# Kernel tuning notes

Hardware: AMD Instinct MI355X
Metric: run time of the kernel (lower is better)

The kernel has to match this reference:

```python
import jax, jax.numpy as jnp
import numpy as np

N = 50000      # nodes
E = 800000     # edges (before self-loops)
NG = 64        # graphs
H, C = 4, 32   # heads, out channels per head
D = 128        # feature dim == H*C
GS, K = 4, 3   # grid_size, spline_order
NB = GS + K    # number of B-spline bases = 7
NC = 10        # classes
L = 3          # gnn layers

# uniform KAN grid over [-1,1] extended by spline_order on each side
GRID = jnp.arange(-K, GS + K + 1, dtype=jnp.float32) * (2.0 / GS) - 1.0  # [GS+2K+1]


def b_splines(x, grid, k):
    # x: [N, in] -> bases: [N, in, GS+k] via Cox-de Boor recursion
    xe = x[..., None]
    bases = ((xe >= grid[:-1]) & (xe < grid[1:])).astype(x.dtype)
    for p in range(1, k + 1):
        left = (xe - grid[:-(p + 1)]) / (grid[p:-1] - grid[:-(p + 1)]) * bases[..., :-1]
        right = (grid[p + 1:] - xe) / (grid[p + 1:] - grid[1:-p]) * bases[..., 1:]
        bases = left + right
    return bases


def kan_linear(x, base_w, spline_w, scaler):
    # efficient-kan: silu(x)@base_w.T + b_splines(x) contracted with scaled spline weights
    base = jax.nn.silu(x) @ base_w.T
    bs = b_splines(x, GRID, K)                      # [N, in, NB]
    sw = spline_w * scaler[..., None]               # [out, in, NB]
    return base + jnp.einsum('nib,oib->no', bs, sw)


def gat_layer(x, src, dst, base_w, spline_w, scaler, att_src, att_dst, bias):
    n = x.shape[0]
    h = kan_linear(x, base_w, spline_w, scaler).reshape(n, H, C)
    a_src = jnp.sum(h * att_src, axis=-1)           # [N, H]
    a_dst = jnp.sum(h * att_dst, axis=-1)           # [N, H]
    e = jax.nn.leaky_relu(a_src[src] + a_dst[dst], 0.2)  # [Etot, H]
    # segment softmax over incoming edges of each destination node
    m = jax.ops.segment_max(e, dst, num_segments=n)
    ex = jnp.exp(e - m[dst])
    s = jax.ops.segment_sum(ex, dst, num_segments=n)
    alpha = ex / (s[dst] + 1e-16)                   # [Etot, H]
    msg = h[src] * alpha[..., None]                 # [Etot, H, C]
    out = jax.ops.segment_sum(msg, dst, num_segments=n)
    return out.reshape(n, H * C) + bias


def setup_inputs() -> dict:
    key = jax.random.key(0)
    ks = jax.random.split(key, 16)
    inp = {
        'x': jax.random.normal(ks[0], (N, D), dtype=jnp.float32),
        'edge_index': jax.random.randint(ks[1], (2, E), 0, N, dtype=jnp.int32),
        'batch': jnp.sort(jax.random.randint(ks[2], (N,), 0, NG, dtype=jnp.int32)),
        # stacked per-layer GAT+KAN params (all layers are [128 -> 128])
        'base_w': jax.random.normal(ks[3], (L, D, D), dtype=jnp.float32) * 0.05,
        'spline_w': jax.random.normal(ks[4], (L, D, D, NB), dtype=jnp.float32) * 0.05,
        'scaler': jax.random.normal(ks[5], (L, D, D), dtype=jnp.float32) * 0.3 + 1.0,
        'att_src': jax.random.normal(ks[6], (L, H, C), dtype=jnp.float32) * 0.1,
        'att_dst': jax.random.normal(ks[7], (L, H, C), dtype=jnp.float32) * 0.1,
        'bias': jnp.zeros((L, H * C), dtype=jnp.float32),
        # readout KANLinear [128 -> 10]
        'ro_base_w': jax.random.normal(ks[8], (NC, D), dtype=jnp.float32) * 0.05,
        'ro_spline_w': jax.random.normal(ks[9], (NC, D, NB), dtype=jnp.float32) * 0.05,
        'ro_scaler': jax.random.normal(ks[10], (NC, D), dtype=jnp.float32) * 0.3 + 1.0,
    }
    return inp


def reference(x, edge_index, batch, base_w, spline_w, scaler, att_src, att_dst, bias,
              ro_base_w, ro_spline_w, ro_scaler):
    # PyG GATConv default: add self-loops
    loops = jnp.arange(N, dtype=edge_index.dtype)
    src = jnp.concatenate([edge_index[0], loops])
    dst = jnp.concatenate([edge_index[1], loops])
    h = x
    for i in range(L):
        h = gat_layer(h, src, dst, base_w[i], spline_w[i], scaler[i],
                      att_src[i], att_dst[i], bias[i])
        h = jax.nn.silu(h)  # dropout is identity in eval mode
    pooled = jax.ops.segment_sum(h, batch, num_segments=NG)   # global_add_pool [NG, D]
    logits = kan_linear(pooled, ro_base_w, ro_spline_w, ro_scaler)
    return jax.nn.log_softmax(logits, axis=1)
```

## Files before the change

### kernel.cpp

```cpp
#include <hip/hip_runtime.h>
#include <math.h>

#define NN 50000
#define EE 800000
#define ETOT (EE + NN)
#define NGR 64
#define DD 128
#define NCL 10

#define NBUK 128
#define BNODES 391
#define P1CH 3321
#define P2CAP 8704

typedef __attribute__((ext_vector_type(16))) float float16_t;
typedef __attribute__((ext_vector_type(8)))  __bf16 bf16x8;

__device__ __forceinline__ float siluf(float x){ return x / (1.f + __expf(-x)); }

__device__ __forceinline__ unsigned f2bf(float f){
  union { float f; unsigned u; } v; v.f = f;
  unsigned r = v.u + 0x7fffu + ((v.u >> 16) & 1u);
  return (r >> 16) & 0xffffu;
}

__device__ __forceinline__ void kan_feats(float x, float* f8){
  f8[0] = siluf(x);
  float u = 2.f*x + 5.f;
  int cell = -1;
  float n0=0.f,n1=0.f,n2=0.f,n3=0.f;
  if (u >= 0.f && u < 10.f){
    cell = (int)u;
    float t = u - (float)cell;
    float t2 = t*t, t3 = t2*t;
    float omt = 1.f - t;
    const float s6 = 1.f/6.f;
    n0 = t3*s6;
    n1 = s6*(1.f + 3.f*t + 3.f*t2 - 3.f*t3);
    n2 = s6*(4.f - 6.f*t2 + 3.f*t3);
    n3 = omt*omt*omt*s6;
  }
#pragma unroll
  for (int j=0;j<7;++j){
    int k = cell - j;
    float v = (k==0)?n0:((k==1)?n1:((k==2)?n2:((k==3)?n3:0.f)));
    f8[1+j] = v;
  }
}

__device__ __forceinline__ int4 kan_feats_pack(float x){
  unsigned sbf = f2bf(siluf(x));
  float u = 2.f*x + 5.f;
  bool valid = (u >= 0.f) && (u < 10.f);
  float uc = valid ? u : 0.f;
  int cell = (int)uc;
  float t = uc - (float)cell;
  float t2 = t*t, t3 = t2*t, omt = 1.f - t;
  const float s6 = 1.f/6.f;
  float n0 = t3*s6;
  float n1 = s6*(1.f + 3.f*t + 3.f*t2 - 3.f*t3);
  float n2 = s6*(4.f - 6.f*t2 + 3.f*t3);
  float n3 = omt*omt*omt*s6;
  unsigned p0=f2bf(n0), p1=f2bf(n1), p2=f2bf(n2), p3=f2bf(n3);
  unsigned long long P = ((unsigned long long)(p1 | (p0<<16)) << 32)
                       |  (unsigned long long)(p3 | (p2<<16));
  int sh = cell*16 - 48;
  unsigned long long shl    = P << (sh & 63);
  unsigned long long shrhi  = P >> ((64 - sh) & 63);
  unsigned long long shllo2 = P << ((sh - 64) & 63);
  unsigned long long shrlo  = P >> ((-sh) & 63);
  unsigned long long F0, F1;
  if (sh < 0)       { F0 = shrlo; F1 = 0ull; }
  else if (sh < 64) { F0 = shl;   F1 = (sh==0)? 0ull : shrhi; }
  else              { F0 = 0ull;  F1 = shllo2; }
  if (!valid){ F0 = 0ull; F1 = 0ull; }
  unsigned w0 = ((unsigned)(F0 & 0xffffull) << 16) | sbf;
  unsigned w1 = (unsigned)((F0 >> 16) & 0xffffffffull);
  unsigned w2 = (unsigned)((F0 >> 48) & 0xffffull) | (((unsigned)(F1 & 0xffffull)) << 16);
  unsigned w3 = (unsigned)((F1 >> 16) & 0xffffffffull);
  return make_int4((int)w0,(int)w1,(int)w2,(int)w3);
}

__global__ void hist_kernel(const int* __restrict__ ei, int* __restrict__ deg){
  int e = blockIdx.x*256 + threadIdx.x;
  if (e >= ETOT) return;
  int dst = (e < EE) ? ei[EE + e] : (e - EE);
  atomicAdd(&deg[dst], 1);
}

__global__ void scan1_kernel(const int* __restrict__ deg, int* __restrict__ offs, int* __restrict__ part){
  __shared__ int sh[256];
  int tid = threadIdx.x;
  int i = blockIdx.x*256 + tid;
  int v = (i < NN) ? deg[i] : 0;
  sh[tid] = v; __syncthreads();
  for (int o=1;o<256;o<<=1){
    int t2 = (tid >= o) ? sh[tid - o] : 0;
    __syncthreads();
    sh[tid] += t2;
    __syncthreads();
  }
  int incl = sh[tid];
  if (i < NN) offs[i] = incl - v;
  if (tid == 255) part[blockIdx.x] = incl;
}

__global__ void scan2_kernel(int* __restrict__ part, int nb){
  __shared__ int sh[256];
  int tid = threadIdx.x;
  int v = (tid < nb) ? part[tid] : 0;
  sh[tid] = v; __syncthreads();
  for (int o=1;o<256;o<<=1){
    int t2 = (tid >= o) ? sh[tid - o] : 0;
    __syncthreads();
    sh[tid] += t2;
    __syncthreads();
  }
  if (tid < nb) part[tid] = sh[tid] - v;
}

__global__ void scan3_kernel(int* __restrict__ offs, const int* __restrict__ part, int* __restrict__ cursor){
  int i = blockIdx.x*256 + threadIdx.x;
  if (i >= NN) return;
  int o = offs[i] + part[blockIdx.x];
  offs[i] = o;
  cursor[i] = o;
}

__global__ void binit_kernel(const int* __restrict__ offs, int* __restrict__ bcur){
  int b = threadIdx.x;
  if (b < NBUK) bcur[b] = offs[b*BNODES];
}

__global__ __launch_bounds__(256) void binpass_kernel(const int* __restrict__ ei,
                                                      int* __restrict__ bcur,
                                                      unsigned* __restrict__ tmp){
  __shared__ int cnt[NBUK], lexcl[NBUK], gbase[NBUK], lcur[NBUK];
  __shared__ int sc[NBUK];
  __shared__ unsigned entries[P1CH + 7];
  const int t = threadIdx.x;
  const int e0 = blockIdx.x * P1CH;
  int e1 = e0 + P1CH; if (e1 > ETOT) e1 = ETOT;
  const int total = e1 - e0;

  if (t < NBUK){ cnt[t] = 0; lcur[t] = 0; }
  __syncthreads();

  unsigned myE[14]; int myB[14]; int myN = 0;
  for (int e = e0 + t; e < e1; e += 256){
    int src, dst;
    if (e < EE){ src = ei[e]; dst = ei[EE + e]; } else { src = e - EE; dst = src; }
    int b = dst / BNODES;
    int dl = dst - b*BNODES;
    myE[myN] = ((unsigned)b << 25) | ((unsigned)dl << 16) | (unsigned)src;
    myB[myN] = b;
    myN++;
    atomicAdd(&cnt[b], 1);
  }
  __syncthreads();

  if (t < NBUK) sc[t] = cnt[t];
  __syncthreads();
  for (int o=1;o<NBUK;o<<=1){
    int v = 0;
    if (t < NBUK && t >= o) v = sc[t - o];
    __syncthreads();
    if (t < NBUK) sc[t] += v;
    __syncthreads();
  }
  if (t < NBUK) lexcl[t] = sc[t] - cnt[t];
  __syncthreads();

  if (t < NBUK && cnt[t] > 0) gbase[t] = atomicAdd(&bcur[t], cnt[t]);
  __syncthreads();

  for (int k=0;k<myN;++k){
    int b = myB[k];
    int r = lexcl[b] + atomicAdd(&lcur[b], 1);
    entries[r] = myE[k];
  }
  __syncthreads();

  for (int s = t; s < total; s += 256){
    unsigned en = entries[s];
    int b = en >> 25;
    int pos = gbase[b] + (s - lexcl[b]);
    tmp[pos] = en;
  }
}

__global__ __launch_bounds__(256) void scatter_kernel(const unsigned* __restrict__ tmp,
                                                      const int* __restrict__ offs,
                                                      int* __restrict__ cursor,
                                                      int* __restrict__ csr){
  __shared__ unsigned ebuf[P2CAP];
  __shared__ unsigned sbuf[P2CAP];
  __shared__ int dcnt[BNODES+1], dscan[BNODES+1], dcur[BNODES+1];
  __shared__ int sA[512], sB[512];
  const int t = threadIdx.x;
  const int b = blockIdx.x;
  const int lo = b * BNODES;
  const int start = offs[lo];
  const int end = (b < NBUK-1) ? offs[lo + BNODES] : ETOT;
  const int cnt = end - start;

  if (cnt > P2CAP){
    for (int i = t; i < cnt; i += 256){
      unsigned en = tmp[start + i];
      int node = lo + (int)((en >> 16) & 0x1FF);
      int pos = atomicAdd(&cursor[node], 1);
      csr[pos] = (int)(en & 0xFFFF);
    }
    return;
  }

  for (int i = t; i < cnt; i += 256) ebuf[i] = tmp[start + i];
  for (int i = t; i < BNODES+1; i += 256){ dcnt[i] = 0; dcur[i] = 0; }
  __syncthreads();
  for (int i = t; i < cnt; i += 256){
    int dl = (ebuf[i] >> 16) & 0x1FF;
    atomicAdd(&dcnt[dl], 1);
  }
  __syncthreads();

  sA[t]       = (t       < BNODES+1) ? dcnt[t]       : 0;
  sA[t + 256] = (t + 256 < BNODES+1) ? dcnt[t + 256] : 0;
  __syncthreads();
  int* sp = sA; int* dp = sB;
  for (int o=1;o<512;o<<=1){
    dp[t]       = sp[t]       + ((t       >= o) ? sp[t - o]       : 0);
    dp[t + 256] = sp[t + 256] + ((t + 256 >= o) ? sp[t + 256 - o] : 0);
    __syncthreads();
    int* tpp = sp; sp = dp; dp = tpp;
  }
  if (t       < BNODES+1) dscan[t]       = sp[t]       - dcnt[t];
  if (t + 256 < BNODES+1) dscan[t + 256] = sp[t + 256] - dcnt[t + 256];
  __syncthreads();

  for (int i = t; i < cnt; i += 256){
    unsigned en = ebuf[i];
    int dl = (en >> 16) & 0x1FF;
    int r = dscan[dl] + atomicAdd(&dcur[dl], 1);
    sbuf[r] = en & 0xFFFFu;
  }
  __syncthreads();
  for (int i = t; i < cnt; i += 256) csr[start + i] = (int)sbuf[i];
}

__global__ void build_wfrag(const float* __restrict__ bw, const float* __restrict__ sw,
                            const float* __restrict__ sc, unsigned short* __restrict__ wfrag){
  int idx = blockIdx.x*256 + threadIdx.x;
  if (idx >= 3*128*1024) return;
  int k = idx & 1023;
  int o = (idx >> 10) & 127;
  int l = idx >> 17;
  int i = k >> 3, f = k & 7;
  int oi = (l*DD + o)*DD + i;
  float w = (f == 0) ? bw[oi] : sw[oi*7 + (f-1)] * sc[oi];
  int s = k >> 6;
  int sl = (k >> 4) & 3, half = (k >> 3) & 1, j = k & 7;
  int ntile = o >> 5, n = o & 31;
  int dst = l*131072 + s*8192 + (((ntile*4 + sl)*64) + half*32 + n)*8 + j;
  wfrag[dst] = (unsigned short)f2bf(w);
}

__global__ __launch_bounds__(256) void kan_gemm(const float* __restrict__ xin,
                                                const unsigned short* __restrict__ wfrag,
                                                const float* __restrict__ attS,
                                                const float* __restrict__ attD,
                                                unsigned int* __restrict__ hpack,
                                                float* __restrict__ asrc,
                                                float* __restrict__ adst, int layer)
{
  __shared__ __align__(16) float xs[64*132];
  __shared__ __align__(16) unsigned short Afrag[2][4096];
  const int t    = threadIdx.x;
  const int lane = t & 63;
  const int w    = t >> 6;
  const int half = lane >> 5;
  const int mn   = lane & 31;
  const int row0 = blockIdx.x * 64;
  const int r_my = t & 63;
  const int il0  = t >> 6;
  const unsigned short* wl = wfrag + layer*131072;

#pragma unroll
  for (int q=0;q<8;++q){
    int p = q*256 + t;
    int r = p >> 5, c4 = p & 31;
    int grow = row0 + r;
    float4 v = make_float4(0.f,0.f,0.f,0.f);
    if (grow < NN) v = *(const float4*)(xin + (size_t)grow*DD + c4*4);
    *(float4*)(&xs[r*132 + c4*4]) = v;
  }
  __syncthreads();

  float16_t acc[2];
#pragma unroll
  for (int i=0;i<16;++i){ acc[0][i]=0.f; acc[1][i]=0.f; }

  int4 Bc[4], Bn[4];
#pragma unroll
  for (int sl=0;sl<4;++sl)
    Bc[sl] = *(const int4*)(wl + ((w*4+sl)*64 + lane)*8);

  const int foa = (((r_my>>5)*8 + il0)*32 + (r_my&31))*8;
  const int fob = (((r_my>>5)*8 + il0+4)*32 + (r_my&31))*8;
  {
    int4 Pa = kan_feats_pack(xs[r_my*132 + il0]);
    int4 Pb = kan_feats_pack(xs[r_my*132 + il0 + 4]);
    *(int4*)(&Afrag[0][foa]) = Pa;
    *(int4*)(&Afrag[0][fob]) = Pb;
  }
  __syncthreads();

  for (int s=0; s<16; ++s){
    if (s < 15){
      const unsigned short* wsrc = wl + (s+1)*8192;
#pragma unroll
      for (int sl=0;sl<4;++sl)
        Bn[sl] = *(const int4*)(wsrc + ((w*4+sl)*64 + lane)*8);
      int4 Pa = kan_feats_pack(xs[r_my*132 + (s+1)*8 + il0]);
      int4 Pb = kan_feats_pack(xs[r_my*132 + (s+1)*8 + il0 + 4]);
      *(int4*)(&Afrag[(s+1)&1][foa]) = Pa;
      *(int4*)(&Afrag[(s+1)&1][fob]) = Pb;
    }
    const unsigned short* A = Afrag[s&1];
#pragma unroll
    for (int sl=0; sl<4; ++sl){
      int4 a0i = *(const int4*)(A + (((0*8 + sl*2 + half)*32) + mn)*8);
      int4 a1i = *(const int4*)(A + (((1*8 + sl*2 + half)*32) + mn)*8);
      bf16x8 b = __builtin_bit_cast(bf16x8, Bc[sl]);
      acc[0] = __builtin_amdgcn_mfma_f32_32x32x16_bf16(__builtin_bit_cast(bf16x8, a0i), b, acc[0], 0, 0, 0);
      acc[1] = __builtin_amdgcn_mfma_f32_32x32x16_bf16(__builtin_bit_cast(bf16x8, a1i), b, acc[1], 0, 0, 0);
    }
#pragma unroll
    for (int sl=0;sl<4;++sl) Bc[sl] = Bn[sl];
    __syncthreads();
  }

  unsigned short* hs = (unsigned short*)xs;
#pragma unroll
  for (int mt=0; mt<2; ++mt){
#pragma unroll
    for (int reg=0; reg<16; ++reg){
      int row = mt*32 + (reg&3) + 8*(reg>>2) + 4*half;
      int col = w*32 + mn;
      hs[row*136 + col] = (unsigned short)f2bf(acc[mt][reg]);
    }
  }
  __syncthreads();
#pragma unroll
  for (int q=0;q<4;++q){
    int p = q*256 + t;
    int row = p >> 4, u4 = p & 15;
    uint4 v = *(const uint4*)((const unsigned int*)(hs + row*136) + u4*4);
    int grow = row0 + row;
    if (grow < NN) *(uint4*)(hpack + (size_t)grow*64 + u4*4) = v;
  }
  {
    int r = t >> 2, h = t & 3;
    const unsigned* hrow = (const unsigned*)(hs + r*136) + h*16;
    const float* ws = attS + (layer*4 + h)*32;
    const float* wd = attD + (layer*4 + h)*32;
    float ss = 0.f, sd = 0.f;
#pragma unroll
    for (int j=0;j<16;++j){
      unsigned u = hrow[j];
      float flo = __uint_as_float(u << 16);
      float fhi = __uint_as_float(u & 0xffff0000u);
      ss += flo*ws[2*j] + fhi*ws[2*j+1];
      sd += flo*wd[2*j] + fhi*wd[2*j+1];
    }
    int grow = row0 + r;
    if (grow < NN){ asrc[grow*4 + h] = ss; adst[grow*4 + h] = sd; }
  }
}

__global__ __launch_bounds__(256) void attn_kernel(
    const unsigned int* __restrict__ hpack, const float* __restrict__ asrc, const float* __restrict__ adst,
    const int* __restrict__ offs, const int* __restrict__ deg, const int* __restrict__ csr,
    const float* __restrict__ bias, float* __restrict__ hout, int layer)
{
  const int wave = threadIdx.x >> 6;
  const int lane = threadIdx.x & 63;
  const int n = blockIdx.x*4 + wave;
  if (n >= NN) return;
  const int st = offs[n];
  const int d  = deg[n];
  const int eL = lane >> 2, h = lane & 3;
  const float adh = adst[n*4 + h];

  int   srcv[4];
  float ev[4];
  float mL = -3.4e38f;
#pragma unroll
  for (int c=0;c<4;++c){
    srcv[c] = 0; ev[c] = -3.4e38f;
    int e = c*16 + eL;
    if (e < d){
      int s2 = csr[st + e];
      srcv[c] = s2;
      float e0 = asrc[s2*4 + h] + adh;
      ev[c] = (e0 > 0.f) ? e0 : 0.2f*e0;
      mL = fmaxf(mL, ev[c]);
    }
  }
  for (int c=64; c<d; c+=16){
    int e = c + eL;
    if (e < d){
      int s2 = csr[st + e];
      float e0 = asrc[s2*4 + h] + adh;
      float evv = (e0 > 0.f) ? e0 : 0.2f*e0;
      mL = fmaxf(mL, evv);
    }
  }
#pragma unroll
  for (int o=4;o<64;o<<=1) mL = fmaxf(mL, __shfl_xor(mL, o));

  float av4[4];
  float sL = 0.f;
#pragma unroll
  for (int c=0;c<4;++c){ av4[c] = __expf(ev[c] - mL); sL += av4[c]; }
  for (int c=64; c<d; c+=16){
    int e = c + eL;
    if (e < d){
      int s2 = csr[st + e];
      float e0 = asrc[s2*4 + h] + adh;
      float evv = (e0 > 0.f) ? e0 : 0.2f*e0;
      sL += __expf(evv - mL);
    }
  }
#pragma unroll
  for (int o=4;o<64;o<<=1) sL += __shfl_xor(sL, o);
  const float inv = 1.f/(sL + 1e-16f);

  const int hq = lane >> 4;
  float accL = 0.f, accH = 0.f;
#pragma unroll
  for (int c=0;c<4;++c){
    if (c*16 < d){
      float ac = av4[c] * inv;
      int lim = d - c*16; if (lim > 16) lim = 16;
      unsigned uv[16]; float aj[16];
#pragma unroll
      for (int j=0;j<16;++j){
        int sj = __shfl(srcv[c], j*4);
        aj[j]  = __shfl(ac,      j*4 + hq);
        if (j < lim) uv[j] = hpack[(size_t)sj*64 + lane];
        else         uv[j] = 0u;
      }
#pragma unroll
      for (int j=0;j<16;++j){
        accL = fmaf(aj[j], __uint_as_float(uv[j] << 16),         accL);
        accH = fmaf(aj[j], __uint_as_float(uv[j] & 0xffff0000u), accH);
      }
    }
  }
  for (int c=64; c<d; c+=16){
    int e = c + eL;
    int s2 = 0; float al = 0.f;
    if (e < d){
      s2 = csr[st + e];
      float e0 = asrc[s2*4 + h] + adh;
      float evv = (e0 > 0.f) ? e0 : 0.2f*e0;
      al = __expf(evv - mL) * inv;
    }
    int lim = d - c; if (lim > 16) lim = 16;
    for (int j=0;j<lim;++j){
      int sj = __shfl(s2, j*4);
      float aH = __shfl(al, j*4 + hq);
      unsigned u = hpack[(size_t)sj*64 + lane];
      accL = fmaf(aH, __uint_as_float(u << 16),         accL);
      accH = fmaf(aH, __uint_as_float(u & 0xffff0000u), accH);
    }
  }
  float2 bv = *(const float2*)(bias + layer*DD + 2*lane);
  float o0 = siluf(accL + bv.x);
  float o1 = siluf(accH + bv.y);
  *(float2*)(hout + (size_t)n*DD + 2*lane) = make_float2(o0, o1);
}

__global__ __launch_bounds__(128) void pool_kernel(const float* __restrict__ h,
    const int* __restrict__ batch, float* __restrict__ pooled)
{
  int c = threadIdx.x;
  int n0 = blockIdx.x*128;
  float sum = 0.f; int cur = -1;
  for (int r=0;r<128;++r){
    int n = n0 + r;
    if (n >= NN) break;
    int g = batch[n];
    if (g != cur){
      if (cur >= 0) atomicAdd(&pooled[cur*DD + c], sum);
      cur = g; sum = 0.f;
    }
    sum += h[n*DD + c];
  }
  if (cur >= 0) atomicAdd(&pooled[cur*DD + c], sum);
}

__global__ __launch_bounds__(64) void readout_kernel(const float* __restrict__ pooled,
    const float* __restrict__ bw, const float* __restrict__ sw, const float* __restrict__ sc,
    float* __restrict__ out)
{
  int g = blockIdx.x, lane = threadIdx.x;
  float xa = pooled[g*DD + lane];
  float xb = pooled[g*DD + lane + 64];
  float fa[8], fb[8];
  kan_feats(xa, fa);
  kan_feats(xb, fb);
  float logits[NCL];
#pragma unroll
  for (int c=0;c<NCL;++c){
    int ia = c*DD + lane, ib = ia + 64;
    float sca = sc[ia], scb = sc[ib];
    float p = fa[0]*bw[ia] + fb[0]*bw[ib];
#pragma unroll
    for (int f=1;f<8;++f)
      p += fa[f]*sw[ia*7 + f-1]*sca + fb[f]*sw[ib*7 + f-1]*scb;
#pragma unroll
    for (int o=1;o<64;o<<=1) p += __shfl_xor(p, o);
    logits[c] = p;
  }
  float mx = logits[0];
#pragma unroll
  for (int c=1;c<NCL;++c) mx = fmaxf(mx, logits[c]);
  float lse = 0.f;
#pragma unroll
  for (int c=0;c<NCL;++c) lse += __expf(logits[c]-mx);
  lse = mx + logf(lse);
  if (lane < NCL){
    float v = 0.f;
#pragma unroll
    for (int c=0;c<NCL;++c) if (lane == c) v = logits[c] - lse;
    out[g*NCL + lane] = v;
  }
}

extern "C" void kernel_launch(void* const* d_in, const int* in_sizes, int n_in,
                              void* d_out, int out_size, void* d_ws, size_t ws_size,
                              hipStream_t stream)
{
  const float* x        = (const float*)d_in[0];
  const int*   ei       = (const int*)  d_in[1];
  const int*   batch    = (const int*)  d_in[2];
  const float* base_w   = (const float*)d_in[3];
  const float* spline_w = (const float*)d_in[4];
  const float* scaler   = (const float*)d_in[5];
  const float* att_src  = (const float*)d_in[6];
  const float* att_dst  = (const float*)d_in[7];
  const float* bias     = (const float*)d_in[8];
  const float* ro_bw    = (const float*)d_in[9];
  const float* ro_sw    = (const float*)d_in[10];
  const float* ro_sc    = (const float*)d_in[11];
  float* out = (float*)d_out;

  char* p = (char*)d_ws;
  auto alloc = [&](size_t bytes)->char* {
    char* r = p;
    p += (bytes + 255) & ~(size_t)255;
    return r;
  };
  unsigned int* hpack = (unsigned int*)alloc((size_t)50048*64*4);
  float* hbuf   = (float*)alloc((size_t)NN*DD*4);
  unsigned short* wfrag = (unsigned short*)alloc((size_t)3*131072*2);
  float* asrc   = (float*)alloc((size_t)NN*4*4);
  float* adst   = (float*)alloc((size_t)NN*4*4);
  float* pooled = (float*)alloc((size_t)NGR*DD*4);
  int*   deg    = (int*)alloc((size_t)NN*4);
  int*   offs   = (int*)alloc((size_t)NN*4);
  int*   cursor = (int*)alloc((size_t)NN*4);
  int*   csr    = (int*)alloc((size_t)ETOT*4);
  unsigned* tmp = (unsigned*)alloc((size_t)ETOT*4);
  int*   bcur   = (int*)alloc((size_t)NBUK*4);
  int*   part   = (int*)alloc((size_t)256*4);

  const int nbs = (NN + 255)/256;
  hipMemsetAsync(deg, 0, (size_t)NN*sizeof(int), stream);
  hist_kernel   <<<(ETOT+255)/256, 256, 0, stream>>>(ei, deg);
  scan1_kernel  <<<nbs, 256, 0, stream>>>(deg, offs, part);
  scan2_kernel  <<<1,   256, 0, stream>>>(part, nbs);
  scan3_kernel  <<<nbs, 256, 0, stream>>>(offs, part, cursor);
  binit_kernel  <<<1,   128, 0, stream>>>(offs, bcur);
  binpass_kernel<<<256, 256, 0, stream>>>(ei, bcur, tmp);
  scatter_kernel<<<NBUK,256, 0, stream>>>(tmp, offs, cursor, csr);
  build_wfrag   <<<(3*128*1024)/256, 256, 0, stream>>>(base_w, spline_w, scaler, wfrag);

  const float* cur = x;
  for (int l=0; l<3; ++l){
    kan_gemm   <<<(NN+63)/64, 256, 0, stream>>>(cur, wfrag, att_src, att_dst,
                                                hpack, asrc, adst, l);
    attn_kernel<<<(NN+3)/4,   256, 0, stream>>>(hpack, asrc, adst, offs, deg, csr,
                                                bias, hbuf, l);
    cur = hbuf;
  }
  hipMemsetAsync(pooled, 0, (size_t)NGR*DD*sizeof(float), stream);
  pool_kernel   <<<(NN+127)/128, 128, 0, stream>>>(hbuf, batch, pooled);
  readout_kernel<<<NGR, 64, 0, stream>>>(pooled, ro_bw, ro_sw, ro_sc, out);
}
```

Baseline: 460.2 us.

## Halve KAN GEMM row tile to 32 and use readlane for uniform source index

The KAN GEMM kernel now processes 32 rows per block instead of 64, with one MFMA accumulator per wave, half the shared memory and a launch-bounds occupancy hint. This doubles the grid size so more blocks are resident, which is meant to hide latency, but the weight fragments are now reloaded for every 32 rows instead of every 64. In the attention kernel, broadcasting the source node index switches from a shuffle to readlane, yielding a scalar value and a scalar-based gather address.

```diff
diff --git a/kernel.cpp b/kernel.cpp
--- a/kernel.cpp
+++ b/kernel.cpp
@@ -264,7 +264,7 @@
   wfrag[dst] = (unsigned short)f2bf(w);
 }
 
-__global__ __launch_bounds__(256) void kan_gemm(const float* __restrict__ xin,
+__global__ __launch_bounds__(256, 6) void kan_gemm(const float* __restrict__ xin,
                                                 const unsigned short* __restrict__ wfrag,
                                                 const float* __restrict__ attS,
                                                 const float* __restrict__ attD,
@@ -272,20 +272,20 @@
                                                 float* __restrict__ asrc,
                                                 float* __restrict__ adst, int layer)
 {
-  __shared__ __align__(16) float xs[64*132];
-  __shared__ __align__(16) unsigned short Afrag[2][4096];
+  __shared__ __align__(16) float xs[32*132];
+  __shared__ __align__(16) unsigned short Afrag[2][2048];
   const int t    = threadIdx.x;
   const int lane = t & 63;
   const int w    = t >> 6;
   const int half = lane >> 5;
   const int mn   = lane & 31;
-  const int row0 = blockIdx.x * 64;
-  const int r_my = t & 63;
-  const int il0  = t >> 6;
+  const int row0 = blockIdx.x * 32;
+  const int r_my = t & 31;
+  const int j_my = t >> 5;
   const unsigned short* wl = wfrag + layer*131072;
 
 #pragma unroll
-  for (int q=0;q<8;++q){
+  for (int q=0;q<4;++q){
     int p = q*256 + t;
     int r = p >> 5, c4 = p & 31;
     int grow = row0 + r;
@@ -295,22 +295,19 @@
   }
   __syncthreads();
 
-  float16_t acc[2];
-#pragma unroll
-  for (int i=0;i<16;++i){ acc[0][i]=0.f; acc[1][i]=0.f; }
+  float16_t acc;
+#pragma unroll
+  for (int i=0;i<16;++i) acc[i]=0.f;
 
   int4 Bc[4], Bn[4];
 #pragma unroll
   for (int sl=0;sl<4;++sl)
     Bc[sl] = *(const int4*)(wl + ((w*4+sl)*64 + lane)*8);
 
-  const int foa = (((r_my>>5)*8 + il0)*32 + (r_my&31))*8;
-  const int fob = (((r_my>>5)*8 + il0+4)*32 + (r_my&31))*8;
+  const int fo = (j_my*32 + r_my)*8;
   {
-    int4 Pa = kan_feats_pack(xs[r_my*132 + il0]);
-    int4 Pb = kan_feats_pack(xs[r_my*132 + il0 + 4]);
-    *(int4*)(&Afrag[0][foa]) = Pa;
-    *(int4*)(&Afrag[0][fob]) = Pb;
+    int4 P = kan_feats_pack(xs[r_my*132 + j_my]);
+    *(int4*)(&Afrag[0][fo]) = P;
   }
   __syncthreads();
 
@@ -320,19 +317,15 @@
 #pragma unroll
       for (int sl=0;sl<4;++sl)
         Bn[sl] = *(const int4*)(wsrc + ((w*4+sl)*64 + lane)*8);
-      int4 Pa = kan_feats_pack(xs[r_my*132 + (s+1)*8 + il0]);
-      int4 Pb = kan_feats_pack(xs[r_my*132 + (s+1)*8 + il0 + 4]);
-      *(int4*)(&Afrag[(s+1)&1][foa]) = Pa;
-      *(int4*)(&Afrag[(s+1)&1][fob]) = Pb;
+      int4 P = kan_feats_pack(xs[r_my*132 + (s+1)*8 + j_my]);
+      *(int4*)(&Afrag[(s+1)&1][fo]) = P;
     }
     const unsigned short* A = Afrag[s&1];
 #pragma unroll
     for (int sl=0; sl<4; ++sl){
-      int4 a0i = *(const int4*)(A + (((0*8 + sl*2 + half)*32) + mn)*8);
-      int4 a1i = *(const int4*)(A + (((1*8 + sl*2 + half)*32) + mn)*8);
+      int4 ai = *(const int4*)(A + ((sl*2 + half)*32 + mn)*8);
       bf16x8 b = __builtin_bit_cast(bf16x8, Bc[sl]);
-      acc[0] = __builtin_amdgcn_mfma_f32_32x32x16_bf16(__builtin_bit_cast(bf16x8, a0i), b, acc[0], 0, 0, 0);
-      acc[1] = __builtin_amdgcn_mfma_f32_32x32x16_bf16(__builtin_bit_cast(bf16x8, a1i), b, acc[1], 0, 0, 0);
+      acc = __builtin_amdgcn_mfma_f32_32x32x16_bf16(__builtin_bit_cast(bf16x8, ai), b, acc, 0, 0, 0);
     }
 #pragma unroll
     for (int sl=0;sl<4;++sl) Bc[sl] = Bn[sl];
@@ -341,24 +334,21 @@
 
   unsigned short* hs = (unsigned short*)xs;
 #pragma unroll
-  for (int mt=0; mt<2; ++mt){
-#pragma unroll
-    for (int reg=0; reg<16; ++reg){
-      int row = mt*32 + (reg&3) + 8*(reg>>2) + 4*half;
-      int col = w*32 + mn;
-      hs[row*136 + col] = (unsigned short)f2bf(acc[mt][reg]);
-    }
-  }
-  __syncthreads();
-#pragma unroll
-  for (int q=0;q<4;++q){
+  for (int reg=0; reg<16; ++reg){
+    int row = (reg&3) + 8*(reg>>2) + 4*half;
+    int col = w*32 + mn;
+    hs[row*136 + col] = (unsigned short)f2bf(acc[reg]);
+  }
+  __syncthreads();
+#pragma unroll
+  for (int q=0;q<2;++q){
     int p = q*256 + t;
     int row = p >> 4, u4 = p & 15;
     uint4 v = *(const uint4*)((const unsigned int*)(hs + row*136) + u4*4);
     int grow = row0 + row;
     if (grow < NN) *(uint4*)(hpack + (size_t)grow*64 + u4*4) = v;
   }
-  {
+  if (t < 128){
     int r = t >> 2, h = t & 3;
     const unsigned* hrow = (const unsigned*)(hs + r*136) + h*16;
     const float* ws = attS + (layer*4 + h)*32;
@@ -445,8 +435,8 @@
       unsigned uv[16]; float aj[16];
 #pragma unroll
       for (int j=0;j<16;++j){
-        int sj = __shfl(srcv[c], j*4);
-        aj[j]  = __shfl(ac,      j*4 + hq);
+        int sj = __builtin_amdgcn_readlane(srcv[c], j*4);
+        aj[j]  = __shfl(ac, j*4 + hq);
         if (j < lim) uv[j] = hpack[(size_t)sj*64 + lane];
         else         uv[j] = 0u;
       }
@@ -468,7 +458,7 @@
     }
     int lim = d - c; if (lim > 16) lim = 16;
     for (int j=0;j<lim;++j){
-      int sj = __shfl(s2, j*4);
+      int sj = __builtin_amdgcn_readlane(s2, j*4);
       float aH = __shfl(al, j*4 + hq);
       unsigned u = hpack[(size_t)sj*64 + lane];
       accL = fmaf(aH, __uint_as_float(u << 16),         accL);
@@ -589,7 +579,7 @@
 
   const float* cur = x;
   for (int l=0; l<3; ++l){
-    kan_gemm   <<<(NN+63)/64, 256, 0, stream>>>(cur, wfrag, att_src, att_dst,
+    kan_gemm   <<<(NN+31)/32, 256, 0, stream>>>(cur, wfrag, att_src, att_dst,
                                                 hpack, asrc, adst, l);
     attn_kernel<<<(NN+3)/4,   256, 0, stream>>>(hpack, asrc, adst, offs, deg, csr,
                                                 bias, hbuf, l);
```

New measurement: 435.1 us. 1.06x faster.
